# Kernel optimization log

Hardware: AMD Instinct MI355X
Metric: run time of the kernel (lower is better)

## Reference

```python
import jax, jax.numpy as jnp
import numpy as np

N, M, E, F = 100000, 20000, 1000000, 128
LEAKY_SLOPE = 0.2
BN_EPS = 1e-5


def segment_softmax(logits, seg, num_segments):
    # numerically stable softmax over ragged segments
    mx = jax.ops.segment_max(logits, seg, num_segments=num_segments)
    mx = jnp.where(jnp.isfinite(mx), mx, 0.0)  # empty segments -> -inf -> 0
    e = jnp.exp(logits - mx[seg])
    s = jax.ops.segment_sum(e, seg, num_segments=num_segments)
    return e / (s[seg] + 1e-16)


def setup_inputs() -> dict:
    key = jax.random.key(0)
    ks = jax.random.split(key, 6)
    return {
        "x": jax.random.normal(ks[0], (N, F), jnp.float32),
        "hyperedge_attr": jax.random.normal(ks[1], (M, F), jnp.float32),
        "W": jax.random.normal(ks[2], (F, F), jnp.float32) / np.sqrt(F),
        "att": jax.random.normal(ks[3], (2 * F,), jnp.float32) * 0.1,
        "bias": jnp.zeros((F,), jnp.float32),
        "gamma": jnp.ones((F,), jnp.float32),
        "beta": jnp.zeros((F,), jnp.float32),
        "node_idx": jax.random.randint(ks[4], (E,), 0, N, dtype=jnp.int32),
        "edge_idx": jax.random.randint(ks[5], (E,), 0, M, dtype=jnp.int32),
    }


def reference(x, hyperedge_attr, W, att, bias, gamma, beta, node_idx, edge_idx):
    # --- HypergraphConv(use_attention=True, heads=1, attention_mode='node') ---
    xw = x @ W                     # [N, F] transformed node features
    ea = hyperedge_attr @ W        # [M, F] transformed hyperedge features (shared lin)

    # per-incidence attention logits: (cat[x_i, e_j] * att).sum(-1)
    a_node = xw @ att[:F]          # [N]
    a_edge = ea @ att[F:]          # [M]
    alpha = a_node[node_idx] + a_edge[edge_idx]          # [E]
    alpha = jax.nn.leaky_relu(alpha, LEAKY_SLOPE)
    alpha = segment_softmax(alpha, edge_idx, M)          # softmax per hyperedge

    ones = jnp.ones((E,), xw.dtype)
    D = jax.ops.segment_sum(ones, node_idx, num_segments=N)   # node degree
    Dinv = jnp.where(D > 0, 1.0 / D, 0.0)
    Bdeg = jax.ops.segment_sum(ones, edge_idx, num_segments=M)  # hyperedge size
    Binv = jnp.where(Bdeg > 0, 1.0 / Bdeg, 0.0)

    # node -> hyperedge: gather node feats, weight by B^{-1}*alpha, scatter to edges
    m1 = (Binv[edge_idx] * alpha)[:, None] * xw[node_idx]        # [E, F]
    edge_feat = jax.ops.segment_sum(m1, edge_idx, num_segments=M)  # [M, F]

    # hyperedge -> node: gather edge feats, weight by D^{-1}*alpha, scatter to nodes
    m2 = (Dinv[node_idx] * alpha)[:, None] * edge_feat[edge_idx]  # [E, F]
    out = jax.ops.segment_sum(m2, node_idx, num_segments=N) + bias  # [N, F]

    # --- BatchNorm1d (training-mode batch statistics, biased variance) ---
    mu = out.mean(axis=0)
    var = out.var(axis=0)
    out = gamma * (out - mu) * jax.lax.rsqrt(var + BN_EPS) + beta

    # --- ELU, dropout (eval: identity), residual (in_dim == out_dim) ---
    out = jax.nn.elu(out)
    return out + x
```

## Files before the change

kernel.cpp:

```cpp
#include <hip/hip_runtime.h>
#include <hip/hip_bf16.h>

#define NN 100000
#define MM 20000
#define EE 1000000
#define FF 128

#define EBK 157
#define NBK 782
#define ECAP 7168
#define NCAP 1664
#define CHUNK 2048
#define NREP 64
#define BM 32

typedef unsigned short u16;
typedef unsigned int u32;
typedef __attribute__((ext_vector_type(8))) short short8v;
typedef __attribute__((ext_vector_type(4))) float f32x4;

__device__ __forceinline__ u16 f2bf(float f) {
  u32 x = __float_as_uint(f);
  return (u16)((x + 0x7FFFu + ((x >> 16) & 1u)) >> 16);
}
__device__ __forceinline__ float bf2f(u16 u) { return __uint_as_float(((u32)u) << 16); }
__device__ __forceinline__ float leaky(float v) { return v > 0.f ? v : 0.2f * v; }
__device__ __forceinline__ float readlane_f(float v, int l) {
  return __uint_as_float((u32)__builtin_amdgcn_readlane((int)__float_as_uint(v), l));
}

__global__ __launch_bounds__(256) void k_prep(const float* __restrict__ W,
                                              const float* __restrict__ att,
                                              float* __restrict__ watt2, u16* __restrict__ WtSwz,
                                              int* __restrict__ ecur, int* __restrict__ ncur,
                                              float* __restrict__ bn_partial) {
  int gid = blockIdx.x * 256 + threadIdx.x;
  if (gid < EBK) ecur[gid] = 0;
  if (gid < NBK) ncur[gid] = 0;
  if (gid < NREP * 256) bn_partial[gid] = 0.f;
  if (blockIdx.x == 0 && threadIdx.x < 128) {
    int t = threadIdx.x;
    float s2 = 0.f;
    for (int c = 0; c < FF; c += 4) {
      float4 wv = *(const float4*)(W + t * FF + c);
      s2 += wv.x * att[FF + c] + wv.y * att[FF + c + 1] + wv.z * att[FF + c + 2] + wv.w * att[FF + c + 3];
    }
    watt2[t] = s2;
    int c = t;
    for (int k = 0; k < FF; k += 2) {
      u32 p = (u32)f2bf(W[k * FF + c]) | ((u32)f2bf(W[(k + 1) * FF + c]) << 16);
      int byte = c * 256 + ((k * 2) ^ ((c & 7) << 4));
      *(u32*)((char*)WtSwz + byte) = p;
    }
  }
}

__global__ __launch_bounds__(256) void k_gemm(const float* __restrict__ x,
                                              const u16* __restrict__ WtSwz,
                                              const float* __restrict__ att,
                                              u16* __restrict__ xw,
                                              float* __restrict__ a_node) {
  __shared__ u16 Wl[FF * FF];
  __shared__ u16 xl[BM * FF];
  __shared__ float pn[BM];
  int t = threadIdx.x;
  {
    const uint4* src = (const uint4*)WtSwz;
    uint4* dst = (uint4*)Wl;
    for (int i = t; i < FF * FF * 2 / 16; i += 256) dst[i] = src[i];
  }
  if (t < BM) pn[t] = 0.f;
  int row0 = blockIdx.x * BM;
  for (int chunk = t; chunk < BM * 32; chunk += 256) {
    int r = chunk >> 5;
    int j = chunk & 31;
    float4 v = ((const float4*)(x + (size_t)(row0 + r) * FF))[j];
    uint2 p;
    p.x = (u32)f2bf(v.x) | ((u32)f2bf(v.y) << 16);
    p.y = (u32)f2bf(v.z) | ((u32)f2bf(v.w) << 16);
    int byte = r * 256 + ((j * 8) ^ ((r & 7) << 4));
    *(uint2*)((char*)xl + byte) = p;
  }
  __syncthreads();

  int wid = t >> 6, lane = t & 63;
  int rt = wid & 1, ch = wid >> 1;
  int r_lo = lane & 15, khalf = lane >> 4;
  f32x4 acc[4];
#pragma unroll
  for (int ct = 0; ct < 4; ++ct) acc[ct] = (f32x4){0.f, 0.f, 0.f, 0.f};

#pragma unroll
  for (int kc = 0; kc < 4; ++kc) {
    int kbyte = kc * 64 + khalf * 16;
    int arow = rt * 16 + r_lo;
    short8v a = *(const short8v*)((const char*)xl + arow * 256 + (kbyte ^ ((arow & 7) << 4)));
#pragma unroll
    for (int ct = 0; ct < 4; ++ct) {
      int brow = ch * 64 + ct * 16 + r_lo;
      short8v b = *(const short8v*)((const char*)Wl + brow * 256 + (kbyte ^ ((brow & 7) << 4)));
      acc[ct] = __builtin_amdgcn_mfma_f32_16x16x32_bf16(a, b, acc[ct], 0, 0, 0);
    }
  }

  float att_c[4];
#pragma unroll
  for (int ct = 0; ct < 4; ++ct) att_c[ct] = att[ch * 64 + ct * 16 + r_lo];
  float p[4] = {0.f, 0.f, 0.f, 0.f};
#pragma unroll
  for (int ct = 0; ct < 4; ++ct) {
#pragma unroll
    for (int reg = 0; reg < 4; ++reg) {
      int lrow = rt * 16 + khalf * 4 + reg;
      xw[(size_t)(row0 + lrow) * FF + ch * 64 + ct * 16 + r_lo] = f2bf(acc[ct][reg]);
      p[reg] += acc[ct][reg] * att_c[ct];
    }
  }
#pragma unroll
  for (int off = 1; off <= 8; off <<= 1) {
#pragma unroll
    for (int reg = 0; reg < 4; ++reg) p[reg] += __shfl_xor(p[reg], off, 64);
  }
  if (r_lo == 0) {
#pragma unroll
    for (int reg = 0; reg < 4; ++reg)
      atomicAdd(&pn[rt * 16 + khalf * 4 + reg], p[reg]);
  }
  __syncthreads();
  if (t < BM) a_node[row0 + t] = pn[t];
}

__global__ __launch_bounds__(256) void k_aedge(const float* __restrict__ he,
                                               const float* __restrict__ watt2,
                                               float* __restrict__ a_edge) {
  int m = (blockIdx.x * 256 + threadIdx.x) >> 6;
  int lane = threadIdx.x & 63;
  if (m >= MM) return;
  float2 wv = ((const float2*)watt2)[lane];
  float2 v = ((const float2*)(he + (size_t)m * FF))[lane];
  float p = v.x * wv.x + v.y * wv.y;
#pragma unroll
  for (int off = 32; off; off >>= 1) p += __shfl_xor(p, off, 64);
  if (lane == 0) a_edge[m] = p;
}

__global__ __launch_bounds__(256) void k_binA(const int* __restrict__ node_idx,
                                              const int* __restrict__ edge_idx,
                                              int* __restrict__ ecur, int* __restrict__ ncur,
                                              u32* __restrict__ ebins, u32* __restrict__ nbins) {
  __shared__ int ecnt[EBK], ncnt[NBK], ebase[EBK], nbase[NBK];
  int t = threadIdx.x;
  for (int i = t; i < EBK; i += 256) ecnt[i] = 0;
  for (int i = t; i < NBK; i += 256) ncnt[i] = 0;
  __syncthreads();
  int start = blockIdx.x * CHUNK;
  int end = min(start + CHUNK, EE);
  for (int e = start + t; e < end; e += 256) {
    int m = edge_idx[e], n = node_idx[e];
    atomicAdd(&ecnt[m >> 7], 1);
    atomicAdd(&ncnt[n >> 7], 1);
  }
  __syncthreads();
  for (int i = t; i < EBK; i += 256) {
    int c = ecnt[i];
    ebase[i] = c ? atomicAdd(&ecur[i], c) : 0;
    ecnt[i] = 0;
  }
  for (int i = t; i < NBK; i += 256) {
    int c = ncnt[i];
    nbase[i] = c ? atomicAdd(&ncur[i], c) : 0;
    ncnt[i] = 0;
  }
  __syncthreads();
  for (int e = start + t; e < end; e += 256) {
    int m = edge_idx[e], n = node_idx[e];
    int eb = m >> 7, nb = n >> 7;
    int p = ebase[eb] + atomicAdd(&ecnt[eb], 1);
    if (p < ECAP) ebins[(size_t)eb * ECAP + p] = ((u32)n << 7) | (u32)(m & 127);
    int q = nbase[nb] + atomicAdd(&ncnt[nb], 1);
    if (q < NCAP) nbins[(size_t)nb * NCAP + q] = ((u32)m << 7) | (u32)(n & 127);
  }
}

__global__ __launch_bounds__(256) void k_binB(const u32* __restrict__ ebins,
                                              const int* __restrict__ ecur,
                                              int* __restrict__ edge_ptr,
                                              int* __restrict__ csrE_node,
                                              float* __restrict__ uwE,
                                              const u32* __restrict__ nbins,
                                              const int* __restrict__ ncur,
                                              int* __restrict__ node_ptr,
                                              int* __restrict__ csrN_edge,
                                              float* __restrict__ uwN,
                                              const float* __restrict__ a_node,
                                              const float* __restrict__ a_edge) {
  __shared__ int cnt[128], cur[128], sc[128];
  __shared__ int ps[256];
  __shared__ float loc[128];
  int t = threadIdx.x;
  bool is_edge = blockIdx.x < EBK;
  int b = is_edge ? blockIdx.x : blockIdx.x - EBK;
  const int* curArr = is_edge ? ecur : ncur;
  const u32* src = is_edge ? (ebins + (size_t)b * ECAP) : (nbins + (size_t)b * NCAP);
  int count = is_edge ? min(ecur[b], ECAP) : min(ncur[b], NCAP);
  int* ptr = is_edge ? edge_ptr : node_ptr;
  int* csr = is_edge ? csrE_node : csrN_edge;
  float* uwArr = is_edge ? uwE : uwN;
  const float* gatherA = is_edge ? a_node : a_edge;
  int glen = is_edge ? MM : NN;
  int nbk = is_edge ? EBK : NBK;

  if (t < 128) {
    int g = b * 128 + t;
    loc[t] = (g < glen) ? (is_edge ? a_edge[g] : a_node[g]) : 0.f;
  }

  int acc = 0;
  for (int i = t; i < b; i += 256) acc += curArr[i];
  ps[t] = acc;
  __syncthreads();
  for (int off = 128; off; off >>= 1) {
    if (t < off) ps[t] += ps[t + off];
    __syncthreads();
  }
  int gbase = ps[0];

  if (t < 128) cnt[t] = 0;
  __syncthreads();
  for (int i = t; i < count; i += 256) atomicAdd(&cnt[src[i] & 127], 1);
  __syncthreads();
  if (t < 128) sc[t] = cnt[t];
  __syncthreads();
  for (int off = 1; off < 128; off <<= 1) {
    int u = (t >= off && t < 128) ? sc[t - off] : 0;
    __syncthreads();
    if (t < 128) sc[t] += u;
    __syncthreads();
  }
  if (t < 128) {
    int excl = sc[t] - cnt[t];
    cur[t] = excl;
    int g = b * 128 + t;
    if (g < glen) ptr[g] = gbase + excl;
  }
  if (b == nbk - 1 && t == 0) ptr[glen] = gbase + count;
  __syncthreads();
  for (int i = t; i < count; i += 256) {
    u32 v = src[i];
    int lo = v & 127;
    int other = (int)(v >> 7);
    int pos = atomicAdd(&cur[lo], 1);
    csr[gbase + pos] = other;
    uwArr[gbase + pos] = __expf(leaky(gatherA[other] + loc[lo]));
  }
}

__global__ __launch_bounds__(256) void k_edge_agg(const int* __restrict__ edge_ptr,
                                                  const int* __restrict__ csrE_node,
                                                  const float* __restrict__ uwE,
                                                  const u16* __restrict__ xw,
                                                  u16* __restrict__ edge_feat,
                                                  float* __restrict__ invsE) {
  int m = (blockIdx.x * 256 + threadIdx.x) >> 6;
  int lane = threadIdx.x & 63;
  if (m >= MM) return;
  int s0 = edge_ptr[m], s1 = edge_ptr[m + 1];
  int len = s1 - s0;
  if (len == 0) return;

  float ssum_l = 0.f;
  float accx = 0.f, accy = 0.f;
  for (int base = s0; base < s1; base += 64) {
    int i = base + lane;
    bool valid = i < s1;
    int n_l = valid ? csrE_node[i] : 0;
    float w_l = valid ? uwE[i] : 0.f;
    ssum_l += w_l;
    int cnt = min(64, s1 - base);
    for (int b = 0; b < cnt; b += 16) {
      u32 u[16];
      float wv[16];
#pragma unroll
      for (int j = 0; j < 16; ++j) {
        int n = __builtin_amdgcn_readlane(n_l, b + j);
        wv[j] = readlane_f(w_l, b + j);
        u[j] = *(const u32*)(xw + (size_t)n * FF + 2 * lane);
      }
#pragma unroll
      for (int j = 0; j < 16; ++j) {
        accx += wv[j] * bf2f((u16)u[j]);
        accy += wv[j] * bf2f((u16)(u[j] >> 16));
      }
    }
  }
#pragma unroll
  for (int off = 1; off < 64; off <<= 1) ssum_l += __shfl_xor(ssum_l, off, 64);
  float invs = 1.0f / (ssum_l + 1e-16f);
  float r = invs / (float)len;
  u32 packed = (u32)f2bf(accx * r) | ((u32)f2bf(accy * r) << 16);
  *(u32*)(edge_feat + (size_t)m * FF + 2 * lane) = packed;
  if (lane == 0) invsE[m] = invs;
}

__global__ __launch_bounds__(256) void k_node_agg(const int* __restrict__ node_ptr,
                                                  const int* __restrict__ csrN_edge,
                                                  const float* __restrict__ uwN,
                                                  const float* __restrict__ invsE,
                                                  const u16* __restrict__ edge_feat,
                                                  const float* __restrict__ bias,
                                                  float* __restrict__ out_f32,
                                                  u16* __restrict__ raw_bf,
                                                  float* __restrict__ bn_partial) {
  __shared__ float4 sd[4][64];
  int wid = threadIdx.x >> 6, lane = threadIdx.x & 63;
  float2 bv = ((const float2*)bias)[lane];
  float s1x = 0.f, s1y = 0.f, s2x = 0.f, s2y = 0.f;
#pragma unroll
  for (int k = 0; k < 4; ++k) {
    int n = blockIdx.x * 16 + wid * 4 + k;
    int s0 = node_ptr[n], s1 = node_ptr[n + 1];
    float accx = 0.f, accy = 0.f;
    for (int base = s0; base < s1; base += 64) {
      int i = base + lane;
      bool valid = i < s1;
      int m_l = valid ? csrN_edge[i] : 0;
      float w_l = valid ? uwN[i] * invsE[m_l] : 0.f;
      int cnt = min(64, s1 - base);
      for (int b = 0; b < cnt; b += 16) {
        u32 u[16];
        float wv[16];
#pragma unroll
        for (int j = 0; j < 16; ++j) {
          int mm = __builtin_amdgcn_readlane(m_l, b + j);
          wv[j] = readlane_f(w_l, b + j);
          u[j] = *(const u32*)(edge_feat + (size_t)mm * FF + 2 * lane);
        }
#pragma unroll
        for (int j = 0; j < 16; ++j) {
          accx += wv[j] * bf2f((u16)u[j]);
          accy += wv[j] * bf2f((u16)(u[j] >> 16));
        }
      }
    }
    int deg = s1 - s0;
    float dinv = deg > 0 ? 1.0f / (float)deg : 0.f;
    float ox = accx * dinv + bv.x;
    float oy = accy * dinv + bv.y;
    if (raw_bf) {
      *(u32*)(raw_bf + (size_t)n * FF + 2 * lane) = (u32)f2bf(ox) | ((u32)f2bf(oy) << 16);
    } else {
      ((float2*)(out_f32 + (size_t)n * FF))[lane] = make_float2(ox, oy);
    }
    s1x += ox; s1y += oy;
    s2x += ox * ox; s2y += oy * oy;
  }
  sd[wid][lane] = make_float4(s1x, s1y, s2x, s2y);
  __syncthreads();
  if (wid == 0) {
    float4 a0 = sd[0][lane], a1 = sd[1][lane], a2 = sd[2][lane], a3 = sd[3][lane];
    float4 s;
    s.x = a0.x + a1.x + a2.x + a3.x;
    s.y = a0.y + a1.y + a2.y + a3.y;
    s.z = a0.z + a1.z + a2.z + a3.z;
    s.w = a0.w + a1.w + a2.w + a3.w;
    float* bp = bn_partial + (blockIdx.x & (NREP - 1)) * 256;
    atomicAdd(bp + 2 * lane, s.x);
    atomicAdd(bp + 2 * lane + 1, s.y);
    atomicAdd(bp + 128 + 2 * lane, s.z);
    atomicAdd(bp + 128 + 2 * lane + 1, s.w);
  }
}

__global__ void k_bn_final(const float* __restrict__ bn_partial, const float* __restrict__ gamma,
                           const float* __restrict__ beta, float* __restrict__ ss) {
  int c = threadIdx.x;
  float s1 = 0.f, s2 = 0.f;
  for (int r = 0; r < NREP; ++r) {
    s1 += bn_partial[r * 256 + c];
    s2 += bn_partial[r * 256 + 128 + c];
  }
  float mu = s1 * (1.0f / NN);
  float var = s2 * (1.0f / NN) - mu * mu;
  var = fmaxf(var, 0.f);
  float sc = gamma[c] * rsqrtf(var + 1e-5f);
  ss[c] = sc;
  ss[FF + c] = beta[c] - mu * sc;
}

__global__ __launch_bounds__(256) void k_finalize(float* __restrict__ out,
                                                  const u16* __restrict__ raw_bf,
                                                  const float* __restrict__ x,
                                                  const float* __restrict__ ss) {
  int idx = blockIdx.x * 256 + threadIdx.x;
  float4 v;
  if (raw_bf) {
    ushort4 rv = *(const ushort4*)(raw_bf + (size_t)idx * 4);
    v = make_float4(bf2f(rv.x), bf2f(rv.y), bf2f(rv.z), bf2f(rv.w));
  } else {
    v = ((const float4*)out)[idx];
  }
  float4 xr = ((const float4*)x)[idx];
  int cb = (idx * 4) & 127;
  float4 sc = *(const float4*)(ss + cb);
  float4 sh = *(const float4*)(ss + FF + cb);
  v.x = fmaf(v.x, sc.x, sh.x);
  v.y = fmaf(v.y, sc.y, sh.y);
  v.z = fmaf(v.z, sc.z, sh.z);
  v.w = fmaf(v.w, sc.w, sh.w);
  v.x = v.x > 0.f ? v.x : expm1f(v.x);
  v.y = v.y > 0.f ? v.y : expm1f(v.y);
  v.z = v.z > 0.f ? v.z : expm1f(v.z);
  v.w = v.w > 0.f ? v.w : expm1f(v.w);
  v.x += xr.x; v.y += xr.y; v.z += xr.z; v.w += xr.w;
  ((float4*)out)[idx] = v;
}

extern "C" void kernel_launch(void* const* d_in, const int* in_sizes, int n_in,
                              void* d_out, int out_size, void* d_ws, size_t ws_size,
                              hipStream_t stream) {
  const float* x     = (const float*)d_in[0];
  const float* he    = (const float*)d_in[1];
  const float* W     = (const float*)d_in[2];
  const float* att   = (const float*)d_in[3];
  const float* bias  = (const float*)d_in[4];
  const float* gamma = (const float*)d_in[5];
  const float* beta  = (const float*)d_in[6];
  const int* node_idx = (const int*)d_in[7];
  const int* edge_idx = (const int*)d_in[8];
  float* out = (float*)d_out;

  char* w = (char*)d_ws;
  auto alloc = [&](size_t bytes) -> char* {
    char* p = w;
    w += (bytes + 255) & ~(size_t)255;
    return p;
  };
  u16*   xw        = (u16*)  alloc((size_t)NN * FF * 2);
  float* a_node    = (float*)alloc((size_t)NN * 4);
  float* a_edge    = (float*)alloc((size_t)MM * 4);
  u16*   WtSwz     = (u16*)  alloc((size_t)FF * FF * 2);
  float* watt2     = (float*)alloc(FF * 4);
  u16*   edge_feat = (u16*)  alloc((size_t)MM * FF * 2);
  float* invsE     = (float*)alloc((size_t)MM * 4);
  int* edge_ptr    = (int*)  alloc((size_t)(MM + 1) * 4);
  int* node_ptr    = (int*)  alloc((size_t)(NN + 1) * 4);
  int* csrE_node   = (int*)  alloc((size_t)EE * 4);
  int* csrN_edge   = (int*)  alloc((size_t)EE * 4);
  float* uwE       = (float*)alloc((size_t)EE * 4);
  float* uwN       = (float*)alloc((size_t)EE * 4);
  int* ecur        = (int*)  alloc((size_t)EBK * 4);
  int* ncur        = (int*)  alloc((size_t)NBK * 4);
  u32* ebins       = (u32*)  alloc((size_t)EBK * ECAP * 4);
  u32* nbins       = (u32*)  alloc((size_t)NBK * NCAP * 4);
  float* bn_partial= (float*)alloc((size_t)NREP * 256 * 4);
  float* ss        = (float*)alloc(2 * FF * 4);
  u16*   raw_cand  = (u16*)  alloc((size_t)NN * FF * 2);
  size_t need = (size_t)(w - (char*)d_ws);
  u16* raw_bf = (need <= ws_size) ? raw_cand : (u16*)nullptr;

  k_prep<<<64, 256, 0, stream>>>(W, att, watt2, WtSwz, ecur, ncur, bn_partial);
  k_gemm<<<NN / BM, 256, 0, stream>>>(x, WtSwz, att, xw, a_node);
  k_aedge<<<(MM * 64 + 255) / 256, 256, 0, stream>>>(he, watt2, a_edge);

  k_binA<<<(EE + CHUNK - 1) / CHUNK, 256, 0, stream>>>(node_idx, edge_idx, ecur, ncur, ebins, nbins);
  k_binB<<<EBK + NBK, 256, 0, stream>>>(ebins, ecur, edge_ptr, csrE_node, uwE,
                                        nbins, ncur, node_ptr, csrN_edge, uwN,
                                        a_node, a_edge);

  k_edge_agg<<<(MM + 3) / 4, 256, 0, stream>>>(edge_ptr, csrE_node, uwE, xw, edge_feat, invsE);
  k_node_agg<<<NN / 16, 256, 0, stream>>>(node_ptr, csrN_edge, uwN, invsE, edge_feat, bias, out, raw_bf, bn_partial);
  k_bn_final<<<1, 128, 0, stream>>>(bn_partial, gamma, beta, ss);
  k_finalize<<<(NN * FF / 4 + 255) / 256, 256, 0, stream>>>(out, raw_bf, x, ss);
}
```

Measured before the change: 202.5 us.

## Pack CSR index and weight into uint2, fold edge normalizer, merge a_edge into gemm

The separate index and weight arrays for both CSR directions are replaced by interleaved uint2 pairs, so each incidence needs one 8-byte load instead of two scattered 4-byte loads. The per-hyperedge softmax normalizer is applied twice when edge_feat is written, which removes the invsE array and its dependent gather in the node aggregation. The a_edge dot-product kernel is merged into the gemm launch as extra blocks to save a kernel launch. In exchange, those extra a_edge blocks still reserve the gemm's large static shared memory, and edge_feat values pick up an extra scaling before bf16 rounding.

Measured after the change: 194.7 us. -3.9%, faster.

```diff
diff --git a/kernel.cpp b/kernel.cpp
--- a/kernel.cpp
+++ b/kernel.cpp
@@ -13,6 +13,8 @@
 #define CHUNK 2048
 #define NREP 64
 #define BM 32
+#define GEMM_BLOCKS (NN / BM)
+#define AEDGE_BLOCKS ((MM + 3) / 4)
 
 typedef unsigned short u16;
 typedef unsigned int u32;
@@ -59,11 +61,28 @@
                                               const u16* __restrict__ WtSwz,
                                               const float* __restrict__ att,
                                               u16* __restrict__ xw,
-                                              float* __restrict__ a_node) {
+                                              float* __restrict__ a_node,
+                                              const float* __restrict__ he,
+                                              const float* __restrict__ watt2,
+                                              float* __restrict__ a_edge) {
   __shared__ u16 Wl[FF * FF];
   __shared__ u16 xl[BM * FF];
   __shared__ float pn[BM];
   int t = threadIdx.x;
+
+  if (blockIdx.x >= GEMM_BLOCKS) {
+    int m = ((blockIdx.x - GEMM_BLOCKS) * 256 + t) >> 6;
+    int lane = t & 63;
+    if (m >= MM) return;
+    float2 wv = ((const float2*)watt2)[lane];
+    float2 v = ((const float2*)(he + (size_t)m * FF))[lane];
+    float p = v.x * wv.x + v.y * wv.y;
+#pragma unroll
+    for (int off = 32; off; off >>= 1) p += __shfl_xor(p, off, 64);
+    if (lane == 0) a_edge[m] = p;
+    return;
+  }
+
   {
     const uint4* src = (const uint4*)WtSwz;
     uint4* dst = (uint4*)Wl;
@@ -130,20 +149,6 @@
   if (t < BM) a_node[row0 + t] = pn[t];
 }
 
-__global__ __launch_bounds__(256) void k_aedge(const float* __restrict__ he,
-                                               const float* __restrict__ watt2,
-                                               float* __restrict__ a_edge) {
-  int m = (blockIdx.x * 256 + threadIdx.x) >> 6;
-  int lane = threadIdx.x & 63;
-  if (m >= MM) return;
-  float2 wv = ((const float2*)watt2)[lane];
-  float2 v = ((const float2*)(he + (size_t)m * FF))[lane];
-  float p = v.x * wv.x + v.y * wv.y;
-#pragma unroll
-  for (int off = 32; off; off >>= 1) p += __shfl_xor(p, off, 64);
-  if (lane == 0) a_edge[m] = p;
-}
-
 __global__ __launch_bounds__(256) void k_binA(const int* __restrict__ node_idx,
                                               const int* __restrict__ edge_idx,
                                               int* __restrict__ ecur, int* __restrict__ ncur,
@@ -185,13 +190,11 @@
 __global__ __launch_bounds__(256) void k_binB(const u32* __restrict__ ebins,
                                               const int* __restrict__ ecur,
                                               int* __restrict__ edge_ptr,
-                                              int* __restrict__ csrE_node,
-                                              float* __restrict__ uwE,
+                                              uint2* __restrict__ pairE,
                                               const u32* __restrict__ nbins,
                                               const int* __restrict__ ncur,
                                               int* __restrict__ node_ptr,
-                                              int* __restrict__ csrN_edge,
-                                              float* __restrict__ uwN,
+                                              uint2* __restrict__ pairN,
                                               const float* __restrict__ a_node,
                                               const float* __restrict__ a_edge) {
   __shared__ int cnt[128], cur[128], sc[128];
@@ -204,8 +207,7 @@
   const u32* src = is_edge ? (ebins + (size_t)b * ECAP) : (nbins + (size_t)b * NCAP);
   int count = is_edge ? min(ecur[b], ECAP) : min(ncur[b], NCAP);
   int* ptr = is_edge ? edge_ptr : node_ptr;
-  int* csr = is_edge ? csrE_node : csrN_edge;
-  float* uwArr = is_edge ? uwE : uwN;
+  uint2* pairArr = is_edge ? pairE : pairN;
   const float* gatherA = is_edge ? a_node : a_edge;
   int glen = is_edge ? MM : NN;
   int nbk = is_edge ? EBK : NBK;
@@ -250,17 +252,15 @@
     int lo = v & 127;
     int other = (int)(v >> 7);
     int pos = atomicAdd(&cur[lo], 1);
-    csr[gbase + pos] = other;
-    uwArr[gbase + pos] = __expf(leaky(gatherA[other] + loc[lo]));
+    float uw = __expf(leaky(gatherA[other] + loc[lo]));
+    pairArr[gbase + pos] = make_uint2((u32)other, __float_as_uint(uw));
   }
 }
 
 __global__ __launch_bounds__(256) void k_edge_agg(const int* __restrict__ edge_ptr,
-                                                  const int* __restrict__ csrE_node,
-                                                  const float* __restrict__ uwE,
+                                                  const uint2* __restrict__ pairE,
                                                   const u16* __restrict__ xw,
-                                                  u16* __restrict__ edge_feat,
-                                                  float* __restrict__ invsE) {
+                                                  u16* __restrict__ edge_feat) {
   int m = (blockIdx.x * 256 + threadIdx.x) >> 6;
   int lane = threadIdx.x & 63;
   if (m >= MM) return;
@@ -273,8 +273,9 @@
   for (int base = s0; base < s1; base += 64) {
     int i = base + lane;
     bool valid = i < s1;
-    int n_l = valid ? csrE_node[i] : 0;
-    float w_l = valid ? uwE[i] : 0.f;
+    uint2 pv = valid ? pairE[i] : make_uint2(0u, 0u);
+    int n_l = (int)pv.x;
+    float w_l = __uint_as_float(pv.y);
     ssum_l += w_l;
     int cnt = min(64, s1 - base);
     for (int b = 0; b < cnt; b += 16) {
@@ -296,16 +297,13 @@
 #pragma unroll
   for (int off = 1; off < 64; off <<= 1) ssum_l += __shfl_xor(ssum_l, off, 64);
   float invs = 1.0f / (ssum_l + 1e-16f);
-  float r = invs / (float)len;
+  float r = invs * invs / (float)len;
   u32 packed = (u32)f2bf(accx * r) | ((u32)f2bf(accy * r) << 16);
   *(u32*)(edge_feat + (size_t)m * FF + 2 * lane) = packed;
-  if (lane == 0) invsE[m] = invs;
 }
 
 __global__ __launch_bounds__(256) void k_node_agg(const int* __restrict__ node_ptr,
-                                                  const int* __restrict__ csrN_edge,
-                                                  const float* __restrict__ uwN,
-                                                  const float* __restrict__ invsE,
+                                                  const uint2* __restrict__ pairN,
                                                   const u16* __restrict__ edge_feat,
                                                   const float* __restrict__ bias,
                                                   float* __restrict__ out_f32,
@@ -323,8 +321,9 @@
     for (int base = s0; base < s1; base += 64) {
       int i = base + lane;
       bool valid = i < s1;
-      int m_l = valid ? csrN_edge[i] : 0;
-      float w_l = valid ? uwN[i] * invsE[m_l] : 0.f;
+      uint2 pv = valid ? pairN[i] : make_uint2(0u, 0u);
+      int m_l = (int)pv.x;
+      float w_l = __uint_as_float(pv.y);
       int cnt = min(64, s1 - base);
       for (int b = 0; b < cnt; b += 16) {
         u32 u[16];
@@ -441,13 +440,10 @@
   u16*   WtSwz     = (u16*)  alloc((size_t)FF * FF * 2);
   float* watt2     = (float*)alloc(FF * 4);
   u16*   edge_feat = (u16*)  alloc((size_t)MM * FF * 2);
-  float* invsE     = (float*)alloc((size_t)MM * 4);
   int* edge_ptr    = (int*)  alloc((size_t)(MM + 1) * 4);
   int* node_ptr    = (int*)  alloc((size_t)(NN + 1) * 4);
-  int* csrE_node   = (int*)  alloc((size_t)EE * 4);
-  int* csrN_edge   = (int*)  alloc((size_t)EE * 4);
-  float* uwE       = (float*)alloc((size_t)EE * 4);
-  float* uwN       = (float*)alloc((size_t)EE * 4);
+  uint2* pairE     = (uint2*)alloc((size_t)EE * 8);
+  uint2* pairN     = (uint2*)alloc((size_t)EE * 8);
   int* ecur        = (int*)  alloc((size_t)EBK * 4);
   int* ncur        = (int*)  alloc((size_t)NBK * 4);
   u32* ebins       = (u32*)  alloc((size_t)EBK * ECAP * 4);
@@ -459,16 +455,16 @@
   u16* raw_bf = (need <= ws_size) ? raw_cand : (u16*)nullptr;
 
   k_prep<<<64, 256, 0, stream>>>(W, att, watt2, WtSwz, ecur, ncur, bn_partial);
-  k_gemm<<<NN / BM, 256, 0, stream>>>(x, WtSwz, att, xw, a_node);
-  k_aedge<<<(MM * 64 + 255) / 256, 256, 0, stream>>>(he, watt2, a_edge);
+  k_gemm<<<GEMM_BLOCKS + AEDGE_BLOCKS, 256, 0, stream>>>(x, WtSwz, att, xw, a_node,
+                                                         he, watt2, a_edge);
 
   k_binA<<<(EE + CHUNK - 1) / CHUNK, 256, 0, stream>>>(node_idx, edge_idx, ecur, ncur, ebins, nbins);
-  k_binB<<<EBK + NBK, 256, 0, stream>>>(ebins, ecur, edge_ptr, csrE_node, uwE,
-                                        nbins, ncur, node_ptr, csrN_edge, uwN,
+  k_binB<<<EBK + NBK, 256, 0, stream>>>(ebins, ecur, edge_ptr, pairE,
+                                        nbins, ncur, node_ptr, pairN,
                                         a_node, a_edge);
 
-  k_edge_agg<<<(MM + 3) / 4, 256, 0, stream>>>(edge_ptr, csrE_node, uwE, xw, edge_feat, invsE);
-  k_node_agg<<<NN / 16, 256, 0, stream>>>(node_ptr, csrN_edge, uwN, invsE, edge_feat, bias, out, raw_bf, bn_partial);
+  k_edge_agg<<<(MM + 3) / 4, 256, 0, stream>>>(edge_ptr, pairE, xw, edge_feat);
+  k_node_agg<<<NN / 16, 256, 0, stream>>>(node_ptr, pairN, edge_feat, bias, out, raw_bf, bn_partial);
   k_bn_final<<<1, 128, 0, stream>>>(bn_partial, gamma, beta, ss);
   k_finalize<<<(NN * FF / 4 + 255) / 256, 256, 0, stream>>>(out, raw_bf, x, ss);
 }
```
